# Kernel tuning notes

Measured on AMD Instinct MI355X. Metric: run time of the kernel, lower is better.

Reference implementation:

```python
import jax, jax.numpy as jnp
import numpy as np
from jax import lax

B, C_IN, H, W = 16, 64, 128, 128
KH, KW, C_OUT = 3, 3, 128


def setup_inputs() -> dict:
    key = jax.random.key(0)
    k1, k2, k3, k4, k5 = jax.random.split(key, 5)
    x = jax.random.normal(k1, (B, C_IN, H, W), jnp.float32)
    # xavier-uniform-ish weight, layout [kh*kw*C_in, C_out] with patch ordering (kh, kw, c)
    limit = np.sqrt(6.0 / (KH * KW * C_IN + C_OUT)).astype(np.float32)
    w = jax.random.uniform(k2, (KH * KW * C_IN, C_OUT), jnp.float32, -limit, limit)
    b = jax.random.uniform(k3, (C_OUT,), jnp.float32)
    q = jax.random.uniform(k4, (1,), jnp.float32)
    p = jax.random.uniform(k5, (1,), jnp.float32)
    return {"x": x, "w": w, "b": b, "q": q, "p": p}


def reference(x, w, b, q, p):
    # Fused implicit-GEMM form of SCS: patch dot products and patch norms are
    # both expressed as convolutions, avoiding the im2col blowup.
    qe = jnp.exp(q[0])
    pe = jnp.exp(p[0])
    # torch patch layout after unfold+moveaxis is (kh, kw, C); w rows follow it
    w_conv = w.reshape(KH, KW, C_IN, C_OUT)  # HWIO
    dn = lax.conv_dimension_numbers(x.shape, w_conv.shape, ('NCHW', 'HWIO', 'NCHW'))
    pad = [(1, 1), (1, 1)]  # pad_len = k-1 = 2, split lo//2, rest (same as torch code)
    # s . k  -> [B, C_out, H, W]
    s_dot_k = lax.conv_general_dilated(x, w_conv, (1, 1), pad, dimension_numbers=dn)
    # ||s||_2 per patch (over kh, kw, C) -> [B, 1, H, W]
    ones_k = jnp.ones((KH, KW, C_IN, 1), x.dtype)
    patch_sq = lax.conv_general_dilated(x * x, ones_k, (1, 1), pad, dimension_numbers=dn)
    norm_s_q = jnp.sqrt(patch_sq) + qe
    norm_k_q = jnp.linalg.norm(w) + qe  # Frobenius norm of the whole weight matrix
    sim = s_dot_k / (norm_s_q * norm_k_q)
    out = jnp.sign(s_dot_k) * jnp.abs(sim) ** pe + b[None, :, None, None]
    return out  # [B, C_out, H, W]
```

## Files before the change

### kernel.cpp

```cpp
#include <hip/hip_runtime.h>
#include <hip/hip_bf16.h>
#include <math.h>

#define B_N 16
#define C_IN 64
#define H_N 128
#define W_N 128
#define C_OUT 128

typedef __attribute__((ext_vector_type(8))) short short8v;
typedef __attribute__((ext_vector_type(4))) float float4v;

__device__ __forceinline__ unsigned short f2bf(float f) {
  union { float f; unsigned u; } c; c.f = f;
  unsigned u = c.u + 0x7fffu + ((c.u >> 16) & 1u);
  return (unsigned short)(u >> 16);
}

__global__ __launch_bounds__(256) void scs_prep_w(
    const float* __restrict__ w, unsigned short* __restrict__ wf,
    float* __restrict__ partial)
{
  __shared__ float red[256];
  const int t    = threadIdx.x;
  const int gid  = blockIdx.x * 256 + t;
  const int frag = gid >> 6;
  const int l    = gid & 63;
  const int kh   = frag / 48;
  const int rem  = frag % 48;
  const int s    = rem >> 3;
  const int nt   = rem & 7;
  const int kb   = kh * 192 + s * 32 + (l >> 4) * 8;
  const int n    = nt * 16 + (l & 15);
  short8v pk;
  float ss = 0.f;
#pragma unroll
  for (int j = 0; j < 8; ++j) {
    const float v = w[(size_t)(kb + j) * C_OUT + n];
    ss = fmaf(v, v, ss);
    pk[j] = (short)f2bf(v);
  }
  *reinterpret_cast<short8v*>(wf + (size_t)frag * 512 + l * 8) = pk;
  red[t] = ss;
  __syncthreads();
  for (int off = 128; off > 0; off >>= 1) {
    if (t < off) red[t] += red[t + off];
    __syncthreads();
  }
  if (t == 0) partial[blockIdx.x] = red[0];
}

#define RS 8448

__global__ __launch_bounds__(512, 6) void scs_main(
    const float* __restrict__ x, const unsigned short* __restrict__ wf,
    const float* __restrict__ bias, const float* __restrict__ q,
    const float* __restrict__ p, const float* __restrict__ partial,
    float* __restrict__ out)
{
  __shared__ alignas(16) char xT[4 * RS];
  __shared__ float psacc[8][4][66];
  __shared__ float pl[2][64];

  const int t   = threadIdx.x;
  const int l   = t & 63;
  const int wid = t >> 6;
  const int wm  = wid >> 2;
  const int wn  = wid & 3;
  const int lr  = l & 15;
  const int lg  = l >> 4;
  const int bid = blockIdx.x;
  const int swz = (bid & 7) * 256 + (bid >> 3);
  const int b   = swz >> 7;
  const int h0  = ((swz >> 1) & 63) << 1;
  const int w0  = (swz & 1) << 6;

  const int wl = t & 63;
  const int g  = t >> 3 & 0;
  const int gg = t >> 6;
  {
    const int jr  = wl + 1;
    int xbyte0 = jr * 128 + gg * 16;
    xbyte0 ^= (jr & 7) << 4;
#pragma unroll
    for (int r = 0; r < 4; ++r) {
      const int  inr   = h0 - 1 + r;
      const bool valid = (unsigned)inr < 128u;
      float ss = 0.f;
      if (valid) {
        const float* src = x + (((size_t)b * C_IN + gg * 8) * H_N + inr) * W_N + w0 + wl;
        float xv[8];
#pragma unroll
        for (int j = 0; j < 8; ++j) xv[j] = src[(size_t)j * H_N * W_N];
#pragma unroll
        for (int j = 0; j < 8; ++j) ss = fmaf(xv[j], xv[j], ss);
        union { __hip_bfloat162 h2[4]; short8v v; } pk;
#pragma unroll
        for (int j = 0; j < 4; ++j)
          pk.h2[j] = __float22bfloat162_rn(make_float2(xv[2 * j], xv[2 * j + 1]));
        *reinterpret_cast<short8v*>(xT + r * RS + xbyte0) = pk.v;
      } else {
        *reinterpret_cast<short8v*>(xT + r * RS + xbyte0) = short8v{0,0,0,0,0,0,0,0};
      }
      psacc[gg][r][jr] = ss;
    }
  }
  if (t < 64) {
    const int e  = t & 1;
    const int r  = (t >> 1) & 3;
    const int g2 = t >> 3;
    const int jr = e ? 65 : 0;
    const int gw = w0 - 1 + e * 65;
    const int inr = h0 - 1 + r;
    const bool valid = ((unsigned)inr < 128u) && ((unsigned)gw < 128u);
    float ss = 0.f;
    int xbyte = r * RS + jr * 128 + g2 * 16;
    xbyte ^= (jr & 7) << 4;
    if (valid) {
      const float* src = x + (((size_t)b * C_IN + g2 * 8) * H_N + inr) * W_N + gw;
      float xv[8];
#pragma unroll
      for (int j = 0; j < 8; ++j) xv[j] = src[(size_t)j * H_N * W_N];
#pragma unroll
      for (int j = 0; j < 8; ++j) ss = fmaf(xv[j], xv[j], ss);
      union { __hip_bfloat162 h2[4]; short8v v; } pk;
#pragma unroll
      for (int j = 0; j < 4; ++j)
        pk.h2[j] = __float22bfloat162_rn(make_float2(xv[2 * j], xv[2 * j + 1]));
      *reinterpret_cast<short8v*>(xT + xbyte) = pk.v;
    } else {
      *reinterpret_cast<short8v*>(xT + xbyte) = short8v{0,0,0,0,0,0,0,0};
    }
    psacc[g2][r][jr] = ss;
  }

  const float bv0 = bias[wn * 32 + lr];
  const float bv1 = bias[wn * 32 + 16 + lr];

  __syncthreads();

  float4v acc[2][2][2];
#pragma unroll
  for (int o = 0; o < 2; ++o)
#pragma unroll
    for (int ml = 0; ml < 2; ++ml)
#pragma unroll
      for (int nl = 0; nl < 2; ++nl) acc[o][ml][nl] = float4v{0.f, 0.f, 0.f, 0.f};

  const int jbase = wm * 32 + lr;
#pragma unroll
  for (int s = 0; s < 6; ++s) {
    const int kw    = s >> 1;
    const int half  = s & 1;
    const int cslot = half * 4 + lg;
    const int jlow  = (lr + kw) & 7;
    const int base_s = (jbase + kw) * 128 + ((cslot * 16) ^ (jlow << 4));

    short8v bfr[3][2];
#pragma unroll
    for (int r = 0; r < 3; ++r) {
      const int fi = (r * 6 + s) * 8 + wn * 2;
      bfr[r][0] = *reinterpret_cast<const short8v*>(wf + (size_t)(fi + 0) * 512 + l * 8);
      bfr[r][1] = *reinterpret_cast<const short8v*>(wf + (size_t)(fi + 1) * 512 + l * 8);
    }
#pragma unroll
    for (int r = 0; r < 4; ++r) {
      short8v a[2];
#pragma unroll
      for (int ml = 0; ml < 2; ++ml)
        a[ml] = *reinterpret_cast<const short8v*>(xT + base_s + r * RS + ml * 2048);
      if (r < 3) {
#pragma unroll
        for (int ml = 0; ml < 2; ++ml)
#pragma unroll
          for (int nl = 0; nl < 2; ++nl)
            acc[0][ml][nl] = __builtin_amdgcn_mfma_f32_16x16x32_bf16(
                a[ml], bfr[r][nl], acc[0][ml][nl], 0, 0, 0);
      }
      if (r >= 1) {
#pragma unroll
        for (int ml = 0; ml < 2; ++ml)
#pragma unroll
          for (int nl = 0; nl < 2; ++nl)
            acc[1][ml][nl] = __builtin_amdgcn_mfma_f32_16x16x32_bf16(
                a[ml], bfr[r - 1][nl], acc[1][ml][nl], 0, 0, 0);
      }
    }
  }

  float ssum = 0.f;
#pragma unroll
  for (int i = 0; i < 36; ++i) ssum += partial[i];
  const float nk = sqrtf(ssum);
  const float qe = __builtin_amdgcn_exp2f(q[0] * 1.4426950408889634f);
  const float pe = __builtin_amdgcn_exp2f(p[0] * 1.4426950408889634f);
  const float nlg_nkq = -__builtin_amdgcn_logf(nk + qe);

  if (t < 128) {
    const int o = t >> 6;
    const int w = t & 63;
    float P = 0.f;
#pragma unroll
    for (int rr = 0; rr < 3; ++rr)
#pragma unroll
      for (int cc = 0; cc < 8; ++cc)
        P += psacc[cc][o + rr][w] + psacc[cc][o + rr][w + 1] + psacc[cc][o + rr][w + 2];
    pl[o][w] = pe * (nlg_nkq - __builtin_amdgcn_logf(sqrtf(P) + qe));
  }
  __syncthreads();

#pragma unroll
  for (int o = 0; o < 2; ++o) {
    const int oh = h0 + o;
#pragma unroll
    for (int ml = 0; ml < 2; ++ml) {
      const int wloc = wm * 32 + ml * 16 + lg * 4;
      const float4v plv = *reinterpret_cast<const float4v*>(&pl[o][wloc]);
#pragma unroll
      for (int nl = 0; nl < 2; ++nl) {
        const int n  = wn * 32 + nl * 16 + lr;
        const float bv = nl ? bv1 : bv0;
        float4v ov;
#pragma unroll
        for (int r = 0; r < 4; ++r) {
          const float sv  = acc[o][ml][nl][r];
          const float lg2 = __builtin_amdgcn_logf(fabsf(sv));
          const float e   = __builtin_amdgcn_exp2f(fmaf(pe, lg2, plv[r]));
          ov[r] = copysignf(e, sv) + bv;
        }
        *reinterpret_cast<float4v*>(
            out + (((size_t)b * C_OUT + n) * H_N + oh) * W_N + w0 + wloc) = ov;
      }
    }
  }
}

extern "C" void kernel_launch(void* const* d_in, const int* in_sizes, int n_in,
                              void* d_out, int out_size, void* d_ws, size_t ws_size,
                              hipStream_t stream) {
  const float* x = (const float*)d_in[0];
  const float* w = (const float*)d_in[1];
  const float* b = (const float*)d_in[2];
  const float* q = (const float*)d_in[3];
  const float* p = (const float*)d_in[4];
  float* out = (float*)d_out;
  float* partial = (float*)d_ws;
  unsigned short* wf = (unsigned short*)((char*)d_ws + 256);

  scs_prep_w<<<36, 256, 0, stream>>>(w, wf, partial);
  scs_main<<<B_N * H_N, 512, 0, stream>>>(x, wf, b, q, p, partial, out);
}
```

Measured before the change: 65.63 us.

## Process 8-row strips per block with a rolling six-row LDS ring and prefetch

Each block now handles an 8-row strip instead of 2 rows, so the grid shrinks from 2048 to 512 blocks. Input rows are kept in a six-slot LDS ring: loads for the next row pair are issued before the MFMA loop and committed after it. This removes the halo re-reading (4 rows loaded per 2 output rows) and overlaps global loads with compute. Patch norms are precomputed per row and summed with a sliding window. In exchange there is more LDS per block, lower occupancy (launch bounds 6 to 4), fewer blocks to fill the CUs, and extra barriers per iteration.

```diff
diff --git a/kernel.cpp b/kernel.cpp
--- a/kernel.cpp
+++ b/kernel.cpp
@@ -7,6 +7,8 @@
 #define H_N 128
 #define W_N 128
 #define C_OUT 128
+#define RS 8448
+#define NSLOT 6
 
 typedef __attribute__((ext_vector_type(8))) short short8v;
 typedef __attribute__((ext_vector_type(4))) float float4v;
@@ -50,17 +52,22 @@
   if (t == 0) partial[blockIdx.x] = red[0];
 }
 
-#define RS 8448
-
-__global__ __launch_bounds__(512, 6) void scs_main(
+#define LGKM_BARRIER()                                   \
+  do {                                                   \
+    asm volatile("s_waitcnt lgkmcnt(0)" ::: "memory");   \
+    __builtin_amdgcn_s_barrier();                        \
+    asm volatile("" ::: "memory");                       \
+  } while (0)
+
+__global__ __launch_bounds__(512, 4) void scs_main(
     const float* __restrict__ x, const unsigned short* __restrict__ wf,
     const float* __restrict__ bias, const float* __restrict__ q,
     const float* __restrict__ p, const float* __restrict__ partial,
     float* __restrict__ out)
 {
-  __shared__ alignas(16) char xT[4 * RS];
-  __shared__ float psacc[8][4][66];
-  __shared__ float pl[2][64];
+  __shared__ alignas(16) char xT[NSLOT * RS];
+  __shared__ float psacc[8][2][66];
+  __shared__ float Ss[NSLOT][66];
 
   const int t   = threadIdx.x;
   const int l   = t & 63;
@@ -70,123 +77,11 @@
   const int lr  = l & 15;
   const int lg  = l >> 4;
   const int bid = blockIdx.x;
-  const int swz = (bid & 7) * 256 + (bid >> 3);
-  const int b   = swz >> 7;
-  const int h0  = ((swz >> 1) & 63) << 1;
-  const int w0  = (swz & 1) << 6;
-
-  const int wl = t & 63;
-  const int g  = t >> 3 & 0;
-  const int gg = t >> 6;
-  {
-    const int jr  = wl + 1;
-    int xbyte0 = jr * 128 + gg * 16;
-    xbyte0 ^= (jr & 7) << 4;
-#pragma unroll
-    for (int r = 0; r < 4; ++r) {
-      const int  inr   = h0 - 1 + r;
-      const bool valid = (unsigned)inr < 128u;
-      float ss = 0.f;
-      if (valid) {
-        const float* src = x + (((size_t)b * C_IN + gg * 8) * H_N + inr) * W_N + w0 + wl;
-        float xv[8];
-#pragma unroll
-        for (int j = 0; j < 8; ++j) xv[j] = src[(size_t)j * H_N * W_N];
-#pragma unroll
-        for (int j = 0; j < 8; ++j) ss = fmaf(xv[j], xv[j], ss);
-        union { __hip_bfloat162 h2[4]; short8v v; } pk;
-#pragma unroll
-        for (int j = 0; j < 4; ++j)
-          pk.h2[j] = __float22bfloat162_rn(make_float2(xv[2 * j], xv[2 * j + 1]));
-        *reinterpret_cast<short8v*>(xT + r * RS + xbyte0) = pk.v;
-      } else {
-        *reinterpret_cast<short8v*>(xT + r * RS + xbyte0) = short8v{0,0,0,0,0,0,0,0};
-      }
-      psacc[gg][r][jr] = ss;
-    }
-  }
-  if (t < 64) {
-    const int e  = t & 1;
-    const int r  = (t >> 1) & 3;
-    const int g2 = t >> 3;
-    const int jr = e ? 65 : 0;
-    const int gw = w0 - 1 + e * 65;
-    const int inr = h0 - 1 + r;
-    const bool valid = ((unsigned)inr < 128u) && ((unsigned)gw < 128u);
-    float ss = 0.f;
-    int xbyte = r * RS + jr * 128 + g2 * 16;
-    xbyte ^= (jr & 7) << 4;
-    if (valid) {
-      const float* src = x + (((size_t)b * C_IN + g2 * 8) * H_N + inr) * W_N + gw;
-      float xv[8];
-#pragma unroll
-      for (int j = 0; j < 8; ++j) xv[j] = src[(size_t)j * H_N * W_N];
-#pragma unroll
-      for (int j = 0; j < 8; ++j) ss = fmaf(xv[j], xv[j], ss);
-      union { __hip_bfloat162 h2[4]; short8v v; } pk;
-#pragma unroll
-      for (int j = 0; j < 4; ++j)
-        pk.h2[j] = __float22bfloat162_rn(make_float2(xv[2 * j], xv[2 * j + 1]));
-      *reinterpret_cast<short8v*>(xT + xbyte) = pk.v;
-    } else {
-      *reinterpret_cast<short8v*>(xT + xbyte) = short8v{0,0,0,0,0,0,0,0};
-    }
-    psacc[g2][r][jr] = ss;
-  }
-
-  const float bv0 = bias[wn * 32 + lr];
-  const float bv1 = bias[wn * 32 + 16 + lr];
-
-  __syncthreads();
-
-  float4v acc[2][2][2];
-#pragma unroll
-  for (int o = 0; o < 2; ++o)
-#pragma unroll
-    for (int ml = 0; ml < 2; ++ml)
-#pragma unroll
-      for (int nl = 0; nl < 2; ++nl) acc[o][ml][nl] = float4v{0.f, 0.f, 0.f, 0.f};
-
-  const int jbase = wm * 32 + lr;
-#pragma unroll
-  for (int s = 0; s < 6; ++s) {
-    const int kw    = s >> 1;
-    const int half  = s & 1;
-    const int cslot = half * 4 + lg;
-    const int jlow  = (lr + kw) & 7;
-    const int base_s = (jbase + kw) * 128 + ((cslot * 16) ^ (jlow << 4));
-
-    short8v bfr[3][2];
-#pragma unroll
-    for (int r = 0; r < 3; ++r) {
-      const int fi = (r * 6 + s) * 8 + wn * 2;
-      bfr[r][0] = *reinterpret_cast<const short8v*>(wf + (size_t)(fi + 0) * 512 + l * 8);
-      bfr[r][1] = *reinterpret_cast<const short8v*>(wf + (size_t)(fi + 1) * 512 + l * 8);
-    }
-#pragma unroll
-    for (int r = 0; r < 4; ++r) {
-      short8v a[2];
-#pragma unroll
-      for (int ml = 0; ml < 2; ++ml)
-        a[ml] = *reinterpret_cast<const short8v*>(xT + base_s + r * RS + ml * 2048);
-      if (r < 3) {
-#pragma unroll
-        for (int ml = 0; ml < 2; ++ml)
-#pragma unroll
-          for (int nl = 0; nl < 2; ++nl)
-            acc[0][ml][nl] = __builtin_amdgcn_mfma_f32_16x16x32_bf16(
-                a[ml], bfr[r][nl], acc[0][ml][nl], 0, 0, 0);
-      }
-      if (r >= 1) {
-#pragma unroll
-        for (int ml = 0; ml < 2; ++ml)
-#pragma unroll
-          for (int nl = 0; nl < 2; ++nl)
-            acc[1][ml][nl] = __builtin_amdgcn_mfma_f32_16x16x32_bf16(
-                a[ml], bfr[r - 1][nl], acc[1][ml][nl], 0, 0, 0);
-      }
-    }
-  }
+  const int swz = (bid & 7) * 64 + (bid >> 3);
+  const int b     = swz >> 5;
+  const int strip = (swz >> 1) & 15;
+  const int w0    = (swz & 1) << 6;
+  const int hs    = strip << 3;
 
   float ssum = 0.f;
 #pragma unroll
@@ -195,43 +90,213 @@
   const float qe = __builtin_amdgcn_exp2f(q[0] * 1.4426950408889634f);
   const float pe = __builtin_amdgcn_exp2f(p[0] * 1.4426950408889634f);
   const float nlg_nkq = -__builtin_amdgcn_logf(nk + qe);
-
-  if (t < 128) {
-    const int o = t >> 6;
-    const int w = t & 63;
-    float P = 0.f;
-#pragma unroll
-    for (int rr = 0; rr < 3; ++rr)
-#pragma unroll
-      for (int cc = 0; cc < 8; ++cc)
-        P += psacc[cc][o + rr][w] + psacc[cc][o + rr][w + 1] + psacc[cc][o + rr][w + 2];
-    pl[o][w] = pe * (nlg_nkq - __builtin_amdgcn_logf(sqrtf(P) + qe));
-  }
-  __syncthreads();
-
-#pragma unroll
-  for (int o = 0; o < 2; ++o) {
-    const int oh = h0 + o;
+  const float bv0 = bias[wn * 32 + lr];
+  const float bv1 = bias[wn * 32 + 16 + lr];
+
+  const int wl = t & 63, gg = t >> 6;
+  const int jr_m    = wl + 1;
+  const int xbyte_m = jr_m * 128 + ((gg * 16) ^ ((jr_m & 7) << 4));
+  const int ee  = t & 1, erp = (t >> 1) & 1, eg = t >> 2;
+  const int e_jr    = ee ? 65 : 0;
+  const int e_gw    = w0 - 1 + ee * 65;
+  const int e_xbyte = e_jr * 128 + ((eg * 16) ^ ((e_jr & 7) << 4));
+
+  float xm[2][8];
+  float xe[8];
+
+#define STAGE_ISSUE(ar0_, ar1_)                                              \
+  {                                                                          \
+    _Pragma("unroll")                                                        \
+    for (int rp = 0; rp < 2; ++rp) {                                         \
+      const int ar_ = rp ? (ar1_) : (ar0_);                                  \
+      if ((unsigned)ar_ < 128u) {                                            \
+        const float* src_ = x + (((size_t)b * C_IN + gg * 8) * H_N + ar_) * W_N + w0 + wl; \
+        _Pragma("unroll")                                                    \
+        for (int j = 0; j < 8; ++j) xm[rp][j] = src_[(size_t)j * H_N * W_N]; \
+      } else {                                                               \
+        _Pragma("unroll")                                                    \
+        for (int j = 0; j < 8; ++j) xm[rp][j] = 0.f;                         \
+      }                                                                      \
+    }                                                                        \
+    if (t < 32) {                                                            \
+      const int ar_ = erp ? (ar1_) : (ar0_);                                 \
+      if (((unsigned)ar_ < 128u) && ((unsigned)e_gw < 128u)) {               \
+        const float* src_ = x + (((size_t)b * C_IN + eg * 8) * H_N + ar_) * W_N + e_gw; \
+        _Pragma("unroll")                                                    \
+        for (int j = 0; j < 8; ++j) xe[j] = src_[(size_t)j * H_N * W_N];     \
+      } else {                                                               \
+        _Pragma("unroll")                                                    \
+        for (int j = 0; j < 8; ++j) xe[j] = 0.f;                             \
+      }                                                                      \
+    }                                                                        \
+  }
+
+#define STAGE_COMMIT(ar0_, ar1_)                                             \
+  {                                                                          \
+    _Pragma("unroll")                                                        \
+    for (int rp = 0; rp < 2; ++rp) {                                         \
+      const int ar_   = rp ? (ar1_) : (ar0_);                                \
+      const int slot_ = (ar_ + 7) % 6;                                       \
+      float ss_ = 0.f;                                                       \
+      _Pragma("unroll")                                                      \
+      for (int j = 0; j < 8; ++j) ss_ = fmaf(xm[rp][j], xm[rp][j], ss_);     \
+      union { __hip_bfloat162 h2[4]; short8v v; } pk_;                       \
+      _Pragma("unroll")                                                      \
+      for (int j = 0; j < 4; ++j)                                            \
+        pk_.h2[j] = __float22bfloat162_rn(make_float2(xm[rp][2*j], xm[rp][2*j+1])); \
+      *reinterpret_cast<short8v*>(xT + slot_ * RS + xbyte_m) = pk_.v;        \
+      psacc[gg][rp][jr_m] = ss_;                                             \
+    }                                                                        \
+    if (t < 32) {                                                            \
+      const int ar_   = erp ? (ar1_) : (ar0_);                               \
+      const int slot_ = (ar_ + 7) % 6;                                       \
+      float ss_ = 0.f;                                                       \
+      _Pragma("unroll")                                                      \
+      for (int j = 0; j < 8; ++j) ss_ = fmaf(xe[j], xe[j], ss_);             \
+      union { __hip_bfloat162 h2[4]; short8v v; } pk_;                       \
+      _Pragma("unroll")                                                      \
+      for (int j = 0; j < 4; ++j)                                            \
+        pk_.h2[j] = __float22bfloat162_rn(make_float2(xe[2*j], xe[2*j+1]));  \
+      *reinterpret_cast<short8v*>(xT + slot_ * RS + e_xbyte) = pk_.v;        \
+      psacc[eg][erp][e_jr] = ss_;                                            \
+    }                                                                        \
+  }
+
+#define REDUCE_SS(ar0_, ar1_)                                                \
+  if (t < 132) {                                                             \
+    const int rp_  = (t >= 66) ? 1 : 0;                                      \
+    const int jr_  = t - 66 * rp_;                                           \
+    const int ar_  = rp_ ? (ar1_) : (ar0_);                                  \
+    const int slot_ = (ar_ + 7) % 6;                                         \
+    float s_ = 0.f;                                                          \
+    _Pragma("unroll")                                                        \
+    for (int g2 = 0; g2 < 8; ++g2) s_ += psacc[g2][rp_][jr_];                \
+    Ss[slot_][jr_] = s_;                                                     \
+  }
+
+  STAGE_ISSUE(hs - 1, hs);
+  STAGE_COMMIT(hs - 1, hs);
+  __syncthreads();
+  REDUCE_SS(hs - 1, hs);
+  STAGE_ISSUE(hs + 1, hs + 2);
+  __syncthreads();
+  STAGE_COMMIT(hs + 1, hs + 2);
+  __syncthreads();
+  REDUCE_SS(hs + 1, hs + 2);
+  __syncthreads();
+
+  const int jbase = wm * 32 + lr;
+#pragma unroll 1
+  for (int hp = 0; hp < 4; ++hp) {
+    const int h0 = hs + 2 * hp;
+    const bool last = (hp == 3);
+
+    if (!last) STAGE_ISSUE(h0 + 3, h0 + 4);
+
+    int soff[4];
+#pragma unroll
+    for (int r = 0; r < 4; ++r) soff[r] = ((h0 + 6 + r) % 6) * RS;
+
+    float4v acc[2][2][2];
+#pragma unroll
+    for (int o = 0; o < 2; ++o)
+#pragma unroll
+      for (int ml = 0; ml < 2; ++ml)
+#pragma unroll
+        for (int nl = 0; nl < 2; ++nl) acc[o][ml][nl] = float4v{0.f, 0.f, 0.f, 0.f};
+
+#pragma unroll
+    for (int s = 0; s < 6; ++s) {
+      const int kw    = s >> 1;
+      const int half  = s & 1;
+      const int cslot = half * 4 + lg;
+      const int jlow  = (lr + kw) & 7;
+      const int base_s = (jbase + kw) * 128 + ((cslot * 16) ^ (jlow << 4));
+      short8v bfr[3][2];
+#pragma unroll
+      for (int r = 0; r < 3; ++r) {
+        const int fi = (r * 6 + s) * 8 + wn * 2;
+        bfr[r][0] = *reinterpret_cast<const short8v*>(wf + (size_t)(fi + 0) * 512 + l * 8);
+        bfr[r][1] = *reinterpret_cast<const short8v*>(wf + (size_t)(fi + 1) * 512 + l * 8);
+      }
+#pragma unroll
+      for (int r = 0; r < 4; ++r) {
+        short8v a[2];
+#pragma unroll
+        for (int ml = 0; ml < 2; ++ml)
+          a[ml] = *reinterpret_cast<const short8v*>(xT + soff[r] + base_s + ml * 2048);
+        if (r < 3) {
+#pragma unroll
+          for (int ml = 0; ml < 2; ++ml)
+#pragma unroll
+            for (int nl = 0; nl < 2; ++nl)
+              acc[0][ml][nl] = __builtin_amdgcn_mfma_f32_16x16x32_bf16(
+                  a[ml], bfr[r][nl], acc[0][ml][nl], 0, 0, 0);
+        }
+        if (r >= 1) {
+#pragma unroll
+          for (int ml = 0; ml < 2; ++ml)
+#pragma unroll
+            for (int nl = 0; nl < 2; ++nl)
+              acc[1][ml][nl] = __builtin_amdgcn_mfma_f32_16x16x32_bf16(
+                  a[ml], bfr[r - 1][nl], acc[1][ml][nl], 0, 0, 0);
+        }
+      }
+    }
+
+    float plr[2][2][4];
 #pragma unroll
     for (int ml = 0; ml < 2; ++ml) {
-      const int wloc = wm * 32 + ml * 16 + lg * 4;
-      const float4v plv = *reinterpret_cast<const float4v*>(&pl[o][wloc]);
-#pragma unroll
-      for (int nl = 0; nl < 2; ++nl) {
-        const int n  = wn * 32 + nl * 16 + lr;
-        const float bv = nl ? bv1 : bv0;
-        float4v ov;
-#pragma unroll
-        for (int r = 0; r < 4; ++r) {
-          const float sv  = acc[o][ml][nl][r];
-          const float lg2 = __builtin_amdgcn_logf(fabsf(sv));
-          const float e   = __builtin_amdgcn_exp2f(fmaf(pe, lg2, plv[r]));
-          ov[r] = copysignf(e, sv) + bv;
+      const int base = wm * 32 + ml * 16 + lg * 4;
+      float cs[4][4];
+#pragma unroll
+      for (int rr = 0; rr < 4; ++rr) {
+        const float* Sr = Ss[(h0 + 6 + rr) % 6];
+        const float v0 = Sr[base],     v1 = Sr[base + 1], v2 = Sr[base + 2];
+        const float v3 = Sr[base + 3], v4 = Sr[base + 4], v5 = Sr[base + 5];
+        cs[rr][0] = v0 + v1 + v2;  cs[rr][1] = v1 + v2 + v3;
+        cs[rr][2] = v2 + v3 + v4;  cs[rr][3] = v3 + v4 + v5;
+      }
+#pragma unroll
+      for (int r = 0; r < 4; ++r) {
+        const float P0 = cs[0][r] + cs[1][r] + cs[2][r];
+        const float P1 = cs[1][r] + cs[2][r] + cs[3][r];
+        plr[0][ml][r] = pe * (nlg_nkq - __builtin_amdgcn_logf(sqrtf(P0) + qe));
+        plr[1][ml][r] = pe * (nlg_nkq - __builtin_amdgcn_logf(sqrtf(P1) + qe));
+      }
+    }
+
+    if (!last) STAGE_COMMIT(h0 + 3, h0 + 4);
+
+    LGKM_BARRIER();
+
+    if (!last) REDUCE_SS(h0 + 3, h0 + 4);
+
+#pragma unroll
+    for (int o = 0; o < 2; ++o) {
+      const int oh = h0 + o;
+#pragma unroll
+      for (int ml = 0; ml < 2; ++ml) {
+        const int wloc = wm * 32 + ml * 16 + lg * 4;
+#pragma unroll
+        for (int nl = 0; nl < 2; ++nl) {
+          const int n  = wn * 32 + nl * 16 + lr;
+          const float bv = nl ? bv1 : bv0;
+          float4v ov;
+#pragma unroll
+          for (int r = 0; r < 4; ++r) {
+            const float sv  = acc[o][ml][nl][r];
+            const float lg2 = __builtin_amdgcn_logf(fabsf(sv));
+            const float e   = __builtin_amdgcn_exp2f(fmaf(pe, lg2, plr[o][ml][r]));
+            ov[r] = copysignf(e, sv) + bv;
+          }
+          *reinterpret_cast<float4v*>(
+              out + (((size_t)b * C_OUT + n) * H_N + oh) * W_N + w0 + wloc) = ov;
         }
-        *reinterpret_cast<float4v*>(
-            out + (((size_t)b * C_OUT + n) * H_N + oh) * W_N + w0 + wloc) = ov;
       }
     }
+
+    LGKM_BARRIER();
   }
 }
 
@@ -248,5 +313,5 @@
   unsigned short* wf = (unsigned short*)((char*)d_ws + 256);
 
   scs_prep_w<<<36, 256, 0, stream>>>(w, wf, partial);
-  scs_main<<<B_N * H_N, 512, 0, stream>>>(x, wf, b, q, p, partial, out);
+  scs_main<<<512, 512, 0, stream>>>(x, wf, b, q, p, partial, out);
 }
```

Measured after the change: 235.5 us. +258.8%, slower.

## Compute four output rows per block to reuse staged input halo rows

Applied to the files above, without the earlier changes.

Each block now covers four output rows instead of two. It stages six input rows into LDS instead of four and keeps four accumulator sets, so every B-fragment load serves up to three output rows. The halo overhead per output row drops (6/4 rows loaded instead of 4/2) and there are half as many blocks. In exchange it uses more LDS and registers and lowers the occupancy hint from 6 to 4, which cuts latency hiding.

```diff
diff --git a/kernel.cpp b/kernel.cpp
--- a/kernel.cpp
+++ b/kernel.cpp
@@ -7,6 +7,7 @@
 #define H_N 128
 #define W_N 128
 #define C_OUT 128
+#define RS 8448
 
 typedef __attribute__((ext_vector_type(8))) short short8v;
 typedef __attribute__((ext_vector_type(4))) float float4v;
@@ -50,17 +51,15 @@
   if (t == 0) partial[blockIdx.x] = red[0];
 }
 
-#define RS 8448
-
-__global__ __launch_bounds__(512, 6) void scs_main(
+__global__ __launch_bounds__(512, 4) void scs_main(
     const float* __restrict__ x, const unsigned short* __restrict__ wf,
     const float* __restrict__ bias, const float* __restrict__ q,
     const float* __restrict__ p, const float* __restrict__ partial,
     float* __restrict__ out)
 {
-  __shared__ alignas(16) char xT[4 * RS];
-  __shared__ float psacc[8][4][66];
-  __shared__ float pl[2][64];
+  __shared__ alignas(16) char xT[6 * RS];
+  __shared__ float psacc[8][6][66];
+  __shared__ float pl[4][64];
 
   const int t   = threadIdx.x;
   const int l   = t & 63;
@@ -70,21 +69,19 @@
   const int lr  = l & 15;
   const int lg  = l >> 4;
   const int bid = blockIdx.x;
-  const int swz = (bid & 7) * 256 + (bid >> 3);
-  const int b   = swz >> 7;
-  const int h0  = ((swz >> 1) & 63) << 1;
-  const int w0  = (swz & 1) << 6;
-
-  const int wl = t & 63;
-  const int g  = t >> 3 & 0;
-  const int gg = t >> 6;
+  const int swz = (bid & 7) * 128 + (bid >> 3);
+  const int b   = swz >> 6;
+  const int rem = swz & 63;
+  const int hs  = (rem >> 1) << 2;
+  const int w0  = (rem & 1) << 6;
+
+  const int wl = t & 63, gg = t >> 6;
   {
-    const int jr  = wl + 1;
-    int xbyte0 = jr * 128 + gg * 16;
-    xbyte0 ^= (jr & 7) << 4;
-#pragma unroll
-    for (int r = 0; r < 4; ++r) {
-      const int  inr   = h0 - 1 + r;
+    const int jr = wl + 1;
+    const int xb = jr * 128 + ((gg * 16) ^ ((jr & 7) << 4));
+#pragma unroll
+    for (int r = 0; r < 6; ++r) {
+      const int  inr   = hs - 1 + r;
       const bool valid = (unsigned)inr < 128u;
       float ss = 0.f;
       if (valid) {
@@ -98,26 +95,26 @@
 #pragma unroll
         for (int j = 0; j < 4; ++j)
           pk.h2[j] = __float22bfloat162_rn(make_float2(xv[2 * j], xv[2 * j + 1]));
-        *reinterpret_cast<short8v*>(xT + r * RS + xbyte0) = pk.v;
+        *reinterpret_cast<short8v*>(xT + r * RS + xb) = pk.v;
       } else {
-        *reinterpret_cast<short8v*>(xT + r * RS + xbyte0) = short8v{0,0,0,0,0,0,0,0};
+        *reinterpret_cast<short8v*>(xT + r * RS + xb) = short8v{0,0,0,0,0,0,0,0};
       }
       psacc[gg][r][jr] = ss;
     }
   }
-  if (t < 64) {
-    const int e  = t & 1;
-    const int r  = (t >> 1) & 3;
-    const int g2 = t >> 3;
-    const int jr = e ? 65 : 0;
-    const int gw = w0 - 1 + e * 65;
-    const int inr = h0 - 1 + r;
+  if (t < 96) {
+    const int re  = t >> 4;
+    const int sub = t & 15;
+    const int ee  = sub & 1;
+    const int ge  = sub >> 1;
+    const int jr  = ee ? 65 : 0;
+    const int gw  = w0 - 1 + ee * 65;
+    const int inr = hs - 1 + re;
     const bool valid = ((unsigned)inr < 128u) && ((unsigned)gw < 128u);
+    const int xb = re * RS + jr * 128 + ((ge * 16) ^ ((jr & 7) << 4));
     float ss = 0.f;
-    int xbyte = r * RS + jr * 128 + g2 * 16;
-    xbyte ^= (jr & 7) << 4;
     if (valid) {
-      const float* src = x + (((size_t)b * C_IN + g2 * 8) * H_N + inr) * W_N + gw;
+      const float* src = x + (((size_t)b * C_IN + ge * 8) * H_N + inr) * W_N + gw;
       float xv[8];
 #pragma unroll
       for (int j = 0; j < 8; ++j) xv[j] = src[(size_t)j * H_N * W_N];
@@ -127,11 +124,11 @@
 #pragma unroll
       for (int j = 0; j < 4; ++j)
         pk.h2[j] = __float22bfloat162_rn(make_float2(xv[2 * j], xv[2 * j + 1]));
-      *reinterpret_cast<short8v*>(xT + xbyte) = pk.v;
+      *reinterpret_cast<short8v*>(xT + xb) = pk.v;
     } else {
-      *reinterpret_cast<short8v*>(xT + xbyte) = short8v{0,0,0,0,0,0,0,0};
-    }
-    psacc[g2][r][jr] = ss;
+      *reinterpret_cast<short8v*>(xT + xb) = short8v{0,0,0,0,0,0,0,0};
+    }
+    psacc[ge][re][jr] = ss;
   }
 
   const float bv0 = bias[wn * 32 + lr];
@@ -139,9 +136,9 @@
 
   __syncthreads();
 
-  float4v acc[2][2][2];
-#pragma unroll
-  for (int o = 0; o < 2; ++o)
+  float4v acc[4][2][2];
+#pragma unroll
+  for (int o = 0; o < 4; ++o)
 #pragma unroll
     for (int ml = 0; ml < 2; ++ml)
 #pragma unroll
@@ -151,39 +148,34 @@
 #pragma unroll
   for (int s = 0; s < 6; ++s) {
     const int kw    = s >> 1;
-    const int half  = s & 1;
-    const int cslot = half * 4 + lg;
+    const int cslot = (s & 1) * 4 + lg;
     const int jlow  = (lr + kw) & 7;
-    const int base_s = (jbase + kw) * 128 + ((cslot * 16) ^ (jlow << 4));
+    const int base_f = (jbase + kw) * 128 + ((cslot * 16) ^ (jlow << 4));
 
     short8v bfr[3][2];
 #pragma unroll
-    for (int r = 0; r < 3; ++r) {
-      const int fi = (r * 6 + s) * 8 + wn * 2;
-      bfr[r][0] = *reinterpret_cast<const short8v*>(wf + (size_t)(fi + 0) * 512 + l * 8);
-      bfr[r][1] = *reinterpret_cast<const short8v*>(wf + (size_t)(fi + 1) * 512 + l * 8);
-    }
-#pragma unroll
-    for (int r = 0; r < 4; ++r) {
+    for (int kh = 0; kh < 3; ++kh) {
+      const int fi = (kh * 6 + s) * 8 + wn * 2;
+      bfr[kh][0] = *reinterpret_cast<const short8v*>(wf + (size_t)(fi + 0) * 512 + l * 8);
+      bfr[kh][1] = *reinterpret_cast<const short8v*>(wf + (size_t)(fi + 1) * 512 + l * 8);
+    }
+#pragma unroll
+    for (int r = 0; r < 6; ++r) {
       short8v a[2];
 #pragma unroll
       for (int ml = 0; ml < 2; ++ml)
-        a[ml] = *reinterpret_cast<const short8v*>(xT + base_s + r * RS + ml * 2048);
-      if (r < 3) {
-#pragma unroll
-        for (int ml = 0; ml < 2; ++ml)
-#pragma unroll
-          for (int nl = 0; nl < 2; ++nl)
-            acc[0][ml][nl] = __builtin_amdgcn_mfma_f32_16x16x32_bf16(
-                a[ml], bfr[r][nl], acc[0][ml][nl], 0, 0, 0);
-      }
-      if (r >= 1) {
-#pragma unroll
-        for (int ml = 0; ml < 2; ++ml)
-#pragma unroll
-          for (int nl = 0; nl < 2; ++nl)
-            acc[1][ml][nl] = __builtin_amdgcn_mfma_f32_16x16x32_bf16(
-                a[ml], bfr[r - 1][nl], acc[1][ml][nl], 0, 0, 0);
+        a[ml] = *reinterpret_cast<const short8v*>(xT + r * RS + base_f + ml * 2048);
+#pragma unroll
+      for (int kh = 0; kh < 3; ++kh) {
+        const int o = r - kh;
+        if (o >= 0 && o < 4) {
+#pragma unroll
+          for (int ml = 0; ml < 2; ++ml)
+#pragma unroll
+            for (int nl = 0; nl < 2; ++nl)
+              acc[o][ml][nl] = __builtin_amdgcn_mfma_f32_16x16x32_bf16(
+                  a[ml], bfr[kh][nl], acc[o][ml][nl], 0, 0, 0);
+        }
       }
     }
   }
@@ -196,22 +188,23 @@
   const float pe = __builtin_amdgcn_exp2f(p[0] * 1.4426950408889634f);
   const float nlg_nkq = -__builtin_amdgcn_logf(nk + qe);
 
-  if (t < 128) {
-    const int o = t >> 6;
-    const int w = t & 63;
+  if (t < 256) {
+    const int o   = t >> 6;
+    const int wl2 = t & 63;
+    const int jc  = wl2 + 1;
     float P = 0.f;
 #pragma unroll
     for (int rr = 0; rr < 3; ++rr)
 #pragma unroll
       for (int cc = 0; cc < 8; ++cc)
-        P += psacc[cc][o + rr][w] + psacc[cc][o + rr][w + 1] + psacc[cc][o + rr][w + 2];
-    pl[o][w] = pe * (nlg_nkq - __builtin_amdgcn_logf(sqrtf(P) + qe));
+        P += psacc[cc][o + rr][jc - 1] + psacc[cc][o + rr][jc] + psacc[cc][o + rr][jc + 1];
+    pl[o][wl2] = pe * (nlg_nkq - __builtin_amdgcn_logf(sqrtf(P) + qe));
   }
   __syncthreads();
 
 #pragma unroll
-  for (int o = 0; o < 2; ++o) {
-    const int oh = h0 + o;
+  for (int o = 0; o < 4; ++o) {
+    const int oh = hs + o;
 #pragma unroll
     for (int ml = 0; ml < 2; ++ml) {
       const int wloc = wm * 32 + ml * 16 + lg * 4;
@@ -248,5 +241,5 @@
   unsigned short* wf = (unsigned short*)((char*)d_ws + 256);
 
   scs_prep_w<<<36, 256, 0, stream>>>(w, wf, partial);
-  scs_main<<<B_N * H_N, 512, 0, stream>>>(x, wf, b, q, p, partial, out);
-}
+  scs_main<<<B_N * (H_N / 4) * 2, 512, 0, stream>>>(x, wf, b, q, p, partial, out);
+}
```

After: 62.35 us. 1.05x faster.
